# Performance work log

Measured on AMD Instinct MI355X. Metric: run time of the kernel, lower is better.

## Reference

```python
import jax, jax.numpy as jnp
import numpy as np

DIM = 1024
N_HEADS = 16
B, T = 2, 2048


def setup_inputs() -> dict:
    key = jax.random.key(0)
    ks = jax.random.split(key, 9)
    s = 1.0 / np.sqrt(DIM)
    return {
        "x": jax.random.normal(ks[0], (B, T, DIM), dtype=jnp.float32),
        "Wq": jax.random.normal(ks[1], (DIM, DIM), dtype=jnp.float32) * s,
        "bq": jnp.zeros((DIM,), dtype=jnp.float32),
        "Wk": jax.random.normal(ks[2], (DIM, DIM), dtype=jnp.float32) * s,
        "bk": jnp.zeros((DIM,), dtype=jnp.float32),
        "Wv": jax.random.normal(ks[3], (DIM, DIM), dtype=jnp.float32) * s,
        "bv": jnp.zeros((DIM,), dtype=jnp.float32),
        "Wo": jax.random.normal(ks[4], (DIM, DIM), dtype=jnp.float32) * s,
        "bo": jnp.zeros((DIM,), dtype=jnp.float32),
    }


def reference(x, Wq, bq, Wk, bk, Wv, bv, Wo, bo):
    Bv, Tv, d = x.shape
    n = N_HEADS
    hd = d // n
    # projections (torch Linear: x @ W.T + b)
    Q = x @ Wq.T + bq
    K = x @ Wk.T + bk
    V = x @ Wv.T + bv
    # [B, n, T, hd]
    Q = Q.reshape(Bv, Tv, n, hd).transpose(0, 2, 1, 3)
    K = K.reshape(Bv, Tv, n, hd).transpose(0, 2, 1, 3)
    V = V.reshape(Bv, Tv, n, hd).transpose(0, 2, 1, 3)
    # NOTE: original scales by full model dim, not head dim
    scale = 1.0 / jnp.sqrt(jnp.asarray(d, dtype=x.dtype))
    scores = jnp.einsum('bnqd,bnkd->bnqk', Q, K) * scale
    causal = jnp.tril(jnp.ones((Tv, Tv), dtype=bool))
    scores = jnp.where(causal, scores, jnp.asarray(-jnp.inf, dtype=scores.dtype))
    attn = jax.nn.softmax(scores, axis=-1)
    out = jnp.einsum('bnqk,bnkd->bnqd', attn, V)
    out = out.transpose(0, 2, 1, 3).reshape(Bv, Tv, d)
    return out @ Wo.T + bo
```

## Files before the change

### kernel.cpp

```cpp
#include <hip/hip_runtime.h>
#include <math.h>

#define DIMN 1024
#define NH 16
#define HD 64
#define BATCH 2
#define SEQ 2048
#define MROWS (BATCH*SEQ)

typedef unsigned short u16;
typedef unsigned int u32;
typedef __attribute__((ext_vector_type(8))) short bf16x8;
typedef __attribute__((ext_vector_type(4))) float f32x4;

__device__ __forceinline__ u16 f2bf(float f) {
    unsigned u = __float_as_uint(f);
    u += 0x7FFF + ((u >> 16) & 1);
    return (u16)(u >> 16);
}
__device__ __forceinline__ float bf2f(u16 s) {
    return __uint_as_float(((unsigned)s) << 16);
}

#define GLOADLDS16(g, s)                                                     \
    __builtin_amdgcn_global_load_lds(                                        \
        (const __attribute__((address_space(1))) void*)(g),                  \
        (__attribute__((address_space(3))) void*)(s), 16, 0, 0)

__global__ __launch_bounds__(256)
void split_hilo(const float* __restrict__ src, u16* __restrict__ h,
                u16* __restrict__ l, int n4)
{
    int i = blockIdx.x * 256 + threadIdx.x;
    if (i >= n4) return;
    float4 v = ((const float4*)src)[i];
    ushort4 hv, lv;
    hv.x = f2bf(v.x); lv.x = f2bf(v.x - bf2f(hv.x));
    hv.y = f2bf(v.y); lv.y = f2bf(v.y - bf2f(hv.y));
    hv.z = f2bf(v.z); lv.z = f2bf(v.z - bf2f(hv.z));
    hv.w = f2bf(v.w); lv.w = f2bf(v.w - bf2f(hv.w));
    ((ushort4*)h)[i] = hv;
    ((ushort4*)l)[i] = lv;
}

#define BM 128
#define BN 128
#define BK 32

template<bool QKV>
__global__ __launch_bounds__(256)
void mfma_gemm(const u16* __restrict__ Ah, const u16* __restrict__ Al,
               const u16* __restrict__ Wh0, const u16* __restrict__ Wl0,
               const u16* __restrict__ Wh1, const u16* __restrict__ Wl1,
               const u16* __restrict__ Wh2, const u16* __restrict__ Wl2,
               const float* __restrict__ b0, const float* __restrict__ b1,
               const float* __restrict__ b2,
               u16* __restrict__ Qh, u16* __restrict__ Ql,
               u16* __restrict__ Kh, u16* __restrict__ Kl,
               float* __restrict__ Vw, float* __restrict__ Yout)
{
    __shared__ u16 AhS[BM*BK], AlS[BM*BK], WhS[BN*BK], WlS[BN*BK];

    const u16* Wh = Wh0; const u16* Wl = Wl0; const float* bias = b0;
    if (QKV) {
        if (blockIdx.z == 1)      { Wh = Wh1; Wl = Wl1; bias = b1; }
        else if (blockIdx.z == 2) { Wh = Wh2; Wl = Wl2; bias = b2; }
    }

    const int tid  = threadIdx.x;
    const int lane = tid & 63;
    const int wid  = tid >> 6;
    const int wr   = wid >> 1;
    const int wc   = wid & 1;

    const int m0 = blockIdx.y * BM;
    const int n0 = blockIdx.x * BN;

    const int srow = lane >> 2;
    const int skc  = (lane & 3) << 3;
    const int c0 = wid * 2, c1 = wid * 2 + 1;
    const size_t aoffg0 = (size_t)(m0 + c0*16 + srow) * DIMN + skc;
    const size_t aoffg1 = (size_t)(m0 + c1*16 + srow) * DIMN + skc;
    const size_t woffg0 = (size_t)(n0 + c0*16 + srow) * DIMN + skc;
    const size_t woffg1 = (size_t)(n0 + c1*16 + srow) * DIMN + skc;

    f32x4 acc[4][4];
    #pragma unroll
    for (int m = 0; m < 4; ++m)
        #pragma unroll
        for (int n = 0; n < 4; ++n)
            acc[m][n] = (f32x4){0.f, 0.f, 0.f, 0.f};

    const int fr = lane & 15;
    const int fq = lane >> 4;
    const int aoff = (wr*64 + fr) * BK + fq*8;
    const int boff = (wc*64 + fr) * BK + fq*8;

    for (int k0 = 0; k0 < DIMN; k0 += BK) {
        GLOADLDS16(Ah + aoffg0 + k0, &AhS[c0*512]);
        GLOADLDS16(Ah + aoffg1 + k0, &AhS[c1*512]);
        GLOADLDS16(Al + aoffg0 + k0, &AlS[c0*512]);
        GLOADLDS16(Al + aoffg1 + k0, &AlS[c1*512]);
        GLOADLDS16(Wh + woffg0 + k0, &WhS[c0*512]);
        GLOADLDS16(Wh + woffg1 + k0, &WhS[c1*512]);
        GLOADLDS16(Wl + woffg0 + k0, &WlS[c0*512]);
        GLOADLDS16(Wl + woffg1 + k0, &WlS[c1*512]);
        __syncthreads();

        bf16x8 ah[4], al[4], bh[4], bl[4];
        #pragma unroll
        for (int m = 0; m < 4; ++m) {
            ah[m] = *(const bf16x8*)&AhS[aoff + m*16*BK];
            al[m] = *(const bf16x8*)&AlS[aoff + m*16*BK];
        }
        #pragma unroll
        for (int n = 0; n < 4; ++n) {
            bh[n] = *(const bf16x8*)&WhS[boff + n*16*BK];
            bl[n] = *(const bf16x8*)&WlS[boff + n*16*BK];
        }
        #pragma unroll
        for (int m = 0; m < 4; ++m)
            #pragma unroll
            for (int n = 0; n < 4; ++n) {
                acc[m][n] = __builtin_amdgcn_mfma_f32_16x16x32_bf16(ah[m], bh[n], acc[m][n], 0, 0, 0);
                acc[m][n] = __builtin_amdgcn_mfma_f32_16x16x32_bf16(ah[m], bl[n], acc[m][n], 0, 0, 0);
                acc[m][n] = __builtin_amdgcn_mfma_f32_16x16x32_bf16(al[m], bh[n], acc[m][n], 0, 0, 0);
            }
        __syncthreads();
    }

    #pragma unroll
    for (int n = 0; n < 4; ++n) {
        const int col = n0 + wc*64 + n*16 + fr;
        const float bv = bias[col];
        #pragma unroll
        for (int m = 0; m < 4; ++m) {
            #pragma unroll
            for (int j = 0; j < 4; ++j) {
                const int row = m0 + wr*64 + m*16 + fq*4 + j;
                float v = acc[m][n][j] + bv;
                if (QKV) {
                    const int b_ = row >> 11, t = row & (SEQ - 1);
                    const int hh = col >> 6, d = col & 63;
                    const size_t rb = (((size_t)b_*NH + hh)*SEQ + t)*HD;
                    if (blockIdx.z == 0) {
                        v *= 0.03125f;
                        u16 hv = f2bf(v), lv = f2bf(v - bf2f(hv));
                        Qh[rb + d] = hv; Ql[rb + d] = lv;
                    } else if (blockIdx.z == 1) {
                        u16 hv = f2bf(v), lv = f2bf(v - bf2f(hv));
                        const int ds = d ^ ((t & 7) << 3);
                        Kh[rb + ds] = hv; Kl[rb + ds] = lv;
                    } else {
                        Vw[rb + d] = v;
                    }
                } else {
                    Yout[(size_t)row*DIMN + col] = v;
                }
            }
        }
    }
}

__global__ __launch_bounds__(256)
void convV(const float* __restrict__ Vw, u16* __restrict__ Vth, u16* __restrict__ Vtl)
{
    __shared__ float Vs[64][68];
    const int tid = threadIdx.x;
    const int bh = blockIdx.y;
    const int t0 = blockIdx.x * 64;
    const float* src = Vw + ((size_t)bh*SEQ + t0)*HD;
    #pragma unroll
    for (int k = 0; k < 4; ++k) {
        int f4 = tid + k*256;
        int r = f4 >> 4, c4 = (f4 & 15) << 2;
        *(float4*)&Vs[r][c4] = *(const float4*)(src + (size_t)r*HD + c4);
    }
    __syncthreads();
    const int d  = tid >> 2;
    const int q2 = (tid & 3) << 4;
    u16* oh = Vth + ((size_t)bh*HD + d)*SEQ + t0;
    u16* ol = Vtl + ((size_t)bh*HD + d)*SEQ + t0;
    #pragma unroll
    for (int p = 0; p < 4; ++p) {
        const int lt = q2 + p*4;
        const int t_sw = (lt & 32) | ((((lt >> 3) & 3) ^ (d & 3)) << 3) | (lt & 7);
        ushort4 hv, lv; float v;
        v = Vs[lt + 0][d]; hv.x = f2bf(v); lv.x = f2bf(v - bf2f(hv.x));
        v = Vs[lt + 1][d]; hv.y = f2bf(v); lv.y = f2bf(v - bf2f(hv.y));
        v = Vs[lt + 2][d]; hv.z = f2bf(v); lv.z = f2bf(v - bf2f(hv.z));
        v = Vs[lt + 3][d]; hv.w = f2bf(v); lv.w = f2bf(v - bf2f(hv.w));
        *(ushort4*)(oh + t_sw) = hv;
        *(ushort4*)(ol + t_sw) = lv;
    }
}

__global__ __launch_bounds__(256)
void attn_mfma(const u16* __restrict__ Qhg, const u16* __restrict__ Qlg,
               const u16* __restrict__ Khg, const u16* __restrict__ Klg,
               const u16* __restrict__ Vthg, const u16* __restrict__ Vtlg,
               u16* __restrict__ AH, u16* __restrict__ AL)
{
    __shared__ u16 KVS[2][4][2048];
    __shared__ u16 PhS[4][640];
    __shared__ u16 PlS[4][640];

    const int tid  = threadIdx.x;
    const int lane = tid & 63;
    const int w    = tid >> 6;
    const int fr   = lane & 15;
    const int fq   = lane >> 4;
    const int bh   = blockIdx.y;
    const int b_   = bh >> 4;
    const int h    = bh & 15;

    auto stage = [&](int buf, int kt2) {
        u16* dst = &KVS[buf][w][0];
        if (w < 2) {
            const u16* g = (w == 0 ? Khg : Klg) +
                ((size_t)bh*SEQ + (size_t)kt2*32 + (lane>>3))*HD + ((lane&7)<<3);
            #pragma unroll
            for (int i = 0; i < 4; ++i)
                GLOADLDS16(g + (size_t)i*8*HD, dst + i*512);
        } else {
            const u16* g = (w == 2 ? Vthg : Vtlg) +
                ((size_t)bh*HD + (lane>>2))*SEQ + (size_t)kt2*32 + ((lane&3)<<3);
            #pragma unroll
            for (int i = 0; i < 4; ++i)
                GLOADLDS16(g + (size_t)i*16*SEQ, dst + i*512);
        }
    };

    #pragma unroll 1
    for (int pass = 0; pass < 2; ++pass) {
        const int qt   = pass ? (31 - blockIdx.x) : blockIdx.x;
        const int qabs = qt*64 + w*16 + fr;
        const int nt   = 2*qt + 2;

        bf16x8 qh[2], ql[2];
        {
            const size_t qrow = ((size_t)bh*SEQ + qabs)*HD;
            #pragma unroll
            for (int ks = 0; ks < 2; ++ks) {
                qh[ks] = *(const bf16x8*)&Qhg[qrow + ks*32 + (fq<<3)];
                ql[ks] = *(const bf16x8*)&Qlg[qrow + ks*32 + (fq<<3)];
            }
        }

        f32x4 o[4];
        #pragma unroll
        for (int md = 0; md < 4; ++md) o[md] = (f32x4){0.f,0.f,0.f,0.f};
        float mrun = -INFINITY, lrun = 0.f;

        __syncthreads();
        stage(0, 0);
        int cur = 0;

        for (int kt = 0; kt < nt; ++kt) {
            __syncthreads();
            if (kt + 1 < nt) stage(cur ^ 1, kt + 1);

            f32x4 s0 = (f32x4){0.f,0.f,0.f,0.f};
            f32x4 s1 = (f32x4){0.f,0.f,0.f,0.f};
            #pragma unroll
            for (int ks = 0; ks < 2; ++ks) {
                const int sl = (((ks*4 + fq) ^ (fr & 7)) << 3);
                bf16x8 a0h = *(const bf16x8*)&KVS[cur][0][fr*64 + sl];
                bf16x8 a0l = *(const bf16x8*)&KVS[cur][1][fr*64 + sl];
                bf16x8 a1h = *(const bf16x8*)&KVS[cur][0][(16+fr)*64 + sl];
                bf16x8 a1l = *(const bf16x8*)&KVS[cur][1][(16+fr)*64 + sl];
                s0 = __builtin_amdgcn_mfma_f32_16x16x32_bf16(a0h, qh[ks], s0, 0,0,0);
                s0 = __builtin_amdgcn_mfma_f32_16x16x32_bf16(a0h, ql[ks], s0, 0,0,0);
                s0 = __builtin_amdgcn_mfma_f32_16x16x32_bf16(a0l, qh[ks], s0, 0,0,0);
                s1 = __builtin_amdgcn_mfma_f32_16x16x32_bf16(a1h, qh[ks], s1, 0,0,0);
                s1 = __builtin_amdgcn_mfma_f32_16x16x32_bf16(a1h, ql[ks], s1, 0,0,0);
                s1 = __builtin_amdgcn_mfma_f32_16x16x32_bf16(a1l, qh[ks], s1, 0,0,0);
            }

            const int kb = kt*32 + fq*4;
            #pragma unroll
            for (int j = 0; j < 4; ++j) {
                if (kb + j      > qabs) s0[j] = -INFINITY;
                if (kb + 16 + j > qabs) s1[j] = -INFINITY;
            }

            float pm = fmaxf(fmaxf(fmaxf(s0[0],s0[1]), fmaxf(s0[2],s0[3])),
                             fmaxf(fmaxf(s1[0],s1[1]), fmaxf(s1[2],s1[3])));
            pm = fmaxf(pm, __shfl_xor(pm, 16));
            pm = fmaxf(pm, __shfl_xor(pm, 32));
            const float mnew = fmaxf(mrun, pm);
            const float fac  = __expf(mrun - mnew);
            float p[8];
            #pragma unroll
            for (int j = 0; j < 4; ++j) {
                p[j]   = __expf(s0[j] - mnew);
                p[4+j] = __expf(s1[j] - mnew);
            }
            float ls = ((p[0]+p[1]) + (p[2]+p[3])) + ((p[4]+p[5]) + (p[6]+p[7]));
            ls += __shfl_xor(ls, 16);
            ls += __shfl_xor(ls, 32);
            lrun = lrun * fac + ls;
            mrun = mnew;
            #pragma unroll
            for (int md = 0; md < 4; ++md) {
                o[md][0] *= fac; o[md][1] *= fac; o[md][2] *= fac; o[md][3] *= fac;
            }

            u16 ph[8], pl[8];
            #pragma unroll
            for (int i = 0; i < 8; ++i) {
                ph[i] = f2bf(p[i]);
                pl[i] = f2bf(p[i] - bf2f(ph[i]));
            }
            {
                const int pb = fr*40 + fq*4;
                uint2 w0, w1;
                w0.x = (u32)ph[0] | ((u32)ph[1] << 16);
                w0.y = (u32)ph[2] | ((u32)ph[3] << 16);
                w1.x = (u32)ph[4] | ((u32)ph[5] << 16);
                w1.y = (u32)ph[6] | ((u32)ph[7] << 16);
                *(uint2*)&PhS[w][pb]      = w0;
                *(uint2*)&PhS[w][pb + 16] = w1;
                w0.x = (u32)pl[0] | ((u32)pl[1] << 16);
                w0.y = (u32)pl[2] | ((u32)pl[3] << 16);
                w1.x = (u32)pl[4] | ((u32)pl[5] << 16);
                w1.y = (u32)pl[6] | ((u32)pl[7] << 16);
                *(uint2*)&PlS[w][pb]      = w0;
                *(uint2*)&PlS[w][pb + 16] = w1;
            }

            bf16x8 bph = *(const bf16x8*)&PhS[w][fr*40 + (fq<<3)];
            bf16x8 bpl = *(const bf16x8*)&PlS[w][fr*40 + (fq<<3)];
            #pragma unroll
            for (int md = 0; md < 4; ++md) {
                const int vsl = ((fq ^ (fr & 3)) << 3);
                bf16x8 avh = *(const bf16x8*)&KVS[cur][2][(md*16+fr)*32 + vsl];
                bf16x8 avl = *(const bf16x8*)&KVS[cur][3][(md*16+fr)*32 + vsl];
                o[md] = __builtin_amdgcn_mfma_f32_16x16x32_bf16(avh, bph, o[md], 0,0,0);
                o[md] = __builtin_amdgcn_mfma_f32_16x16x32_bf16(avh, bpl, o[md], 0,0,0);
                o[md] = __builtin_amdgcn_mfma_f32_16x16x32_bf16(avl, bph, o[md], 0,0,0);
            }
            cur ^= 1;
        }

        const float inv = 1.f / lrun;
        const size_t ob = ((size_t)b_*SEQ + qabs)*DIMN + h*64;
        #pragma unroll
        for (int md = 0; md < 4; ++md) {
            #pragma unroll
            for (int pr = 0; pr < 2; ++pr) {
                const int d0 = md*16 + fq*4 + pr*2;
                const float v0 = o[md][pr*2]   * inv;
                const float v1 = o[md][pr*2+1] * inv;
                u16 h0 = f2bf(v0), l0 = f2bf(v0 - bf2f(h0));
                u16 h1 = f2bf(v1), l1 = f2bf(v1 - bf2f(h1));
                *(u32*)&AH[ob + d0] = (u32)h0 | ((u32)h1 << 16);
                *(u32*)&AL[ob + d0] = (u32)l0 | ((u32)l1 << 16);
            }
        }
    }
}

extern "C" void kernel_launch(void* const* d_in, const int* in_sizes, int n_in,
                              void* d_out, int out_size, void* d_ws, size_t ws_size,
                              hipStream_t stream)
{
    const float* x  = (const float*)d_in[0];
    const float* Wq = (const float*)d_in[1];
    const float* bq = (const float*)d_in[2];
    const float* Wk = (const float*)d_in[3];
    const float* bk = (const float*)d_in[4];
    const float* Wv = (const float*)d_in[5];
    const float* bv = (const float*)d_in[6];
    const float* Wo = (const float*)d_in[7];
    const float* bo = (const float*)d_in[8];
    float* out = (float*)d_out;

    const size_t NX = (size_t)MROWS * DIMN;
    const size_t NW = (size_t)DIMN * DIMN;

    u16* Xh  = (u16*)d_ws;
    u16* Xl  = Xh  + NX;
    u16* WhQ = Xl  + NX;
    u16* WlQ = WhQ + NW;
    u16* WhK = WlQ + NW;
    u16* WlK = WhK + NW;
    u16* WhV = WlK + NW;
    u16* WlV = WhV + NW;
    u16* WhO = WlV + NW;
    u16* WlO = WhO + NW;
    u16* Qh  = WlO + NW;
    u16* Ql  = Qh + NX;
    u16* Kh  = Ql + NX;
    u16* Kl  = Kh + NX;
    u16* Vth = Kl + NX;
    u16* Vtl = Vth + NX;
    float* Vw = (float*)(Vtl + NX);
    u16* AH = Xh;
    u16* AL = Xl;

    const int n4x = (int)(NX / 4);
    const int n4w = (int)(NW / 4);
    split_hilo<<<n4x/256, 256, 0, stream>>>(x,  Xh,  Xl,  n4x);
    split_hilo<<<n4w/256, 256, 0, stream>>>(Wq, WhQ, WlQ, n4w);
    split_hilo<<<n4w/256, 256, 0, stream>>>(Wk, WhK, WlK, n4w);
    split_hilo<<<n4w/256, 256, 0, stream>>>(Wv, WhV, WlV, n4w);
    split_hilo<<<n4w/256, 256, 0, stream>>>(Wo, WhO, WlO, n4w);

    dim3 gq(DIMN / BN, MROWS / BM, 3);
    mfma_gemm<true><<<gq, 256, 0, stream>>>(Xh, Xl, WhQ, WlQ, WhK, WlK, WhV, WlV,
                                            bq, bk, bv, Qh, Ql, Kh, Kl, Vw, nullptr);

    dim3 gv(SEQ / 64, BATCH * NH);
    convV<<<gv, 256, 0, stream>>>(Vw, Vth, Vtl);

    dim3 ga(16, BATCH * NH);
    attn_mfma<<<ga, 256, 0, stream>>>(Qh, Ql, Kh, Kl, Vth, Vtl, AH, AL);

    dim3 gp(DIMN / BN, MROWS / BM, 1);
    mfma_gemm<false><<<gp, 256, 0, stream>>>(AH, AL, WhO, WlO, nullptr, nullptr,
                                             nullptr, nullptr, bo, nullptr, nullptr,
                                             nullptr, nullptr, nullptr, nullptr,
                                             nullptr, out);
}
```

Before: 380.2 us.

## Pre-pack operands into MFMA fragment order and drop LDS staging in GEMMs

The hi/lo bf16 split kernel now writes x and the weights in a packed layout that matches the MFMA 16x32 fragment order. Each wave can then load its fragments straight from global memory with contiguous 16-byte loads, so the GEMM no longer stages through LDS and no longer needs the block barriers. The attention kernel now writes fp32 output, and a separate pack pass converts it before the output projection, which uses a narrower 4x2 fragment tile per wave to give a larger grid. This adds an extra pass over the attention output. It also gives up LDS reuse between the waves of a block, so more traffic must be served by L2.

```diff
diff --git a/kernel.cpp b/kernel.cpp
--- a/kernel.cpp
+++ b/kernel.cpp
@@ -7,6 +7,7 @@
 #define BATCH 2
 #define SEQ 2048
 #define MROWS (BATCH*SEQ)
+#define NKB   (DIMN/32)
 
 typedef unsigned short u16;
 typedef unsigned int u32;
@@ -28,43 +29,50 @@
         (__attribute__((address_space(3))) void*)(s), 16, 0, 0)
 
 __global__ __launch_bounds__(256)
-void split_hilo(const float* __restrict__ src, u16* __restrict__ h,
-                u16* __restrict__ l, int n4)
+void pack_hilo(const float* __restrict__ src, u16* __restrict__ dh,
+               u16* __restrict__ dl, int ngran)
 {
-    int i = blockIdx.x * 256 + threadIdx.x;
-    if (i >= n4) return;
-    float4 v = ((const float4*)src)[i];
-    ushort4 hv, lv;
-    hv.x = f2bf(v.x); lv.x = f2bf(v.x - bf2f(hv.x));
-    hv.y = f2bf(v.y); lv.y = f2bf(v.y - bf2f(hv.y));
-    hv.z = f2bf(v.z); lv.z = f2bf(v.z - bf2f(hv.z));
-    hv.w = f2bf(v.w); lv.w = f2bf(v.w - bf2f(hv.w));
-    ((ushort4*)h)[i] = hv;
-    ((ushort4*)l)[i] = lv;
-}
-
-#define BM 128
-#define BN 128
-#define BK 32
-
-template<bool QKV>
+    int g = blockIdx.x * 256 + threadIdx.x;
+    if (g >= ngran) return;
+    const int lane = g & 63;
+    const int kb   = (g >> 6) & (NKB - 1);
+    const int rb   = g >> 11;
+    const int row  = rb * 16 + (lane & 15);
+    const int col  = kb * 32 + (lane >> 4) * 8;
+    const float* s = src + (size_t)row * DIMN + col;
+    float4 v0 = *(const float4*)s;
+    float4 v1 = *(const float4*)(s + 4);
+    ushort4 h0, h1, l0, l1;
+    h0.x = f2bf(v0.x); l0.x = f2bf(v0.x - bf2f(h0.x));
+    h0.y = f2bf(v0.y); l0.y = f2bf(v0.y - bf2f(h0.y));
+    h0.z = f2bf(v0.z); l0.z = f2bf(v0.z - bf2f(h0.z));
+    h0.w = f2bf(v0.w); l0.w = f2bf(v0.w - bf2f(h0.w));
+    h1.x = f2bf(v1.x); l1.x = f2bf(v1.x - bf2f(h1.x));
+    h1.y = f2bf(v1.y); l1.y = f2bf(v1.y - bf2f(h1.y));
+    h1.z = f2bf(v1.z); l1.z = f2bf(v1.z - bf2f(h1.z));
+    h1.w = f2bf(v1.w); l1.w = f2bf(v1.w - bf2f(h1.w));
+    *(ushort4*)(dh + (size_t)g * 8)     = h0;
+    *(ushort4*)(dh + (size_t)g * 8 + 4) = h1;
+    *(ushort4*)(dl + (size_t)g * 8)     = l0;
+    *(ushort4*)(dl + (size_t)g * 8 + 4) = l1;
+}
+
+template<int MF, int NF, bool QKV>
 __global__ __launch_bounds__(256)
-void mfma_gemm(const u16* __restrict__ Ah, const u16* __restrict__ Al,
-               const u16* __restrict__ Wh0, const u16* __restrict__ Wl0,
-               const u16* __restrict__ Wh1, const u16* __restrict__ Wl1,
-               const u16* __restrict__ Wh2, const u16* __restrict__ Wl2,
-               const float* __restrict__ b0, const float* __restrict__ b1,
-               const float* __restrict__ b2,
-               u16* __restrict__ Qh, u16* __restrict__ Ql,
-               u16* __restrict__ Kh, u16* __restrict__ Kl,
-               float* __restrict__ Vw, float* __restrict__ Yout)
+void pgemm(const u16* __restrict__ Aph, const u16* __restrict__ Apl,
+           const u16* __restrict__ Wph0, const u16* __restrict__ Wpl0,
+           const u16* __restrict__ Wph1, const u16* __restrict__ Wpl1,
+           const u16* __restrict__ Wph2, const u16* __restrict__ Wpl2,
+           const float* __restrict__ b0, const float* __restrict__ b1,
+           const float* __restrict__ b2,
+           u16* __restrict__ Qh, u16* __restrict__ Ql,
+           u16* __restrict__ Kh, u16* __restrict__ Kl,
+           float* __restrict__ Vw, float* __restrict__ Yout)
 {
-    __shared__ u16 AhS[BM*BK], AlS[BM*BK], WhS[BN*BK], WlS[BN*BK];
-
-    const u16* Wh = Wh0; const u16* Wl = Wl0; const float* bias = b0;
+    const u16* Wph = Wph0; const u16* Wpl = Wpl0; const float* bias = b0;
     if (QKV) {
-        if (blockIdx.z == 1)      { Wh = Wh1; Wl = Wl1; bias = b1; }
-        else if (blockIdx.z == 2) { Wh = Wh2; Wl = Wl2; bias = b2; }
+        if (blockIdx.z == 1)      { Wph = Wph1; Wpl = Wpl1; bias = b1; }
+        else if (blockIdx.z == 2) { Wph = Wph2; Wpl = Wpl2; bias = b2; }
     }
 
     const int tid  = threadIdx.x;
@@ -72,72 +80,55 @@
     const int wid  = tid >> 6;
     const int wr   = wid >> 1;
     const int wc   = wid & 1;
-
-    const int m0 = blockIdx.y * BM;
-    const int n0 = blockIdx.x * BN;
-
-    const int srow = lane >> 2;
-    const int skc  = (lane & 3) << 3;
-    const int c0 = wid * 2, c1 = wid * 2 + 1;
-    const size_t aoffg0 = (size_t)(m0 + c0*16 + srow) * DIMN + skc;
-    const size_t aoffg1 = (size_t)(m0 + c1*16 + srow) * DIMN + skc;
-    const size_t woffg0 = (size_t)(n0 + c0*16 + srow) * DIMN + skc;
-    const size_t woffg1 = (size_t)(n0 + c1*16 + srow) * DIMN + skc;
-
-    f32x4 acc[4][4];
+    const int mb0  = blockIdx.y * (2*MF) + wr*MF;
+    const int nb0  = blockIdx.x * (2*NF) + wc*NF;
+
+    const u16* Ah = Aph + (size_t)mb0 * (NKB*512) + lane*8;
+    const u16* Al = Apl + (size_t)mb0 * (NKB*512) + lane*8;
+    const u16* Bh = Wph + (size_t)nb0 * (NKB*512) + lane*8;
+    const u16* Bl = Wpl + (size_t)nb0 * (NKB*512) + lane*8;
+
+    f32x4 acc[MF][NF];
     #pragma unroll
-    for (int m = 0; m < 4; ++m)
-        #pragma unroll
-        for (int n = 0; n < 4; ++n)
+    for (int m = 0; m < MF; ++m)
+        #pragma unroll
+        for (int n = 0; n < NF; ++n)
             acc[m][n] = (f32x4){0.f, 0.f, 0.f, 0.f};
 
-    const int fr = lane & 15;
-    const int fq = lane >> 4;
-    const int aoff = (wr*64 + fr) * BK + fq*8;
-    const int boff = (wc*64 + fr) * BK + fq*8;
-
-    for (int k0 = 0; k0 < DIMN; k0 += BK) {
-        GLOADLDS16(Ah + aoffg0 + k0, &AhS[c0*512]);
-        GLOADLDS16(Ah + aoffg1 + k0, &AhS[c1*512]);
-        GLOADLDS16(Al + aoffg0 + k0, &AlS[c0*512]);
-        GLOADLDS16(Al + aoffg1 + k0, &AlS[c1*512]);
-        GLOADLDS16(Wh + woffg0 + k0, &WhS[c0*512]);
-        GLOADLDS16(Wh + woffg1 + k0, &WhS[c1*512]);
-        GLOADLDS16(Wl + woffg0 + k0, &WlS[c0*512]);
-        GLOADLDS16(Wl + woffg1 + k0, &WlS[c1*512]);
-        __syncthreads();
-
-        bf16x8 ah[4], al[4], bh[4], bl[4];
-        #pragma unroll
-        for (int m = 0; m < 4; ++m) {
-            ah[m] = *(const bf16x8*)&AhS[aoff + m*16*BK];
-            al[m] = *(const bf16x8*)&AlS[aoff + m*16*BK];
-        }
-        #pragma unroll
-        for (int n = 0; n < 4; ++n) {
-            bh[n] = *(const bf16x8*)&WhS[boff + n*16*BK];
-            bl[n] = *(const bf16x8*)&WlS[boff + n*16*BK];
-        }
-        #pragma unroll
-        for (int m = 0; m < 4; ++m)
-            #pragma unroll
-            for (int n = 0; n < 4; ++n) {
+    for (int kb = 0; kb < NKB; ++kb) {
+        const int ko = kb * 512;
+        bf16x8 ah[MF], al[MF], bh[NF], bl[NF];
+        #pragma unroll
+        for (int m = 0; m < MF; ++m) {
+            ah[m] = *(const bf16x8*)(Ah + ko + m*(NKB*512));
+            al[m] = *(const bf16x8*)(Al + ko + m*(NKB*512));
+        }
+        #pragma unroll
+        for (int n = 0; n < NF; ++n) {
+            bh[n] = *(const bf16x8*)(Bh + ko + n*(NKB*512));
+            bl[n] = *(const bf16x8*)(Bl + ko + n*(NKB*512));
+        }
+        #pragma unroll
+        for (int m = 0; m < MF; ++m)
+            #pragma unroll
+            for (int n = 0; n < NF; ++n) {
                 acc[m][n] = __builtin_amdgcn_mfma_f32_16x16x32_bf16(ah[m], bh[n], acc[m][n], 0, 0, 0);
                 acc[m][n] = __builtin_amdgcn_mfma_f32_16x16x32_bf16(ah[m], bl[n], acc[m][n], 0, 0, 0);
                 acc[m][n] = __builtin_amdgcn_mfma_f32_16x16x32_bf16(al[m], bh[n], acc[m][n], 0, 0, 0);
             }
-        __syncthreads();
-    }
-
+    }
+
+    const int fr = lane & 15;
+    const int fq = lane >> 4;
     #pragma unroll
-    for (int n = 0; n < 4; ++n) {
-        const int col = n0 + wc*64 + n*16 + fr;
+    for (int n = 0; n < NF; ++n) {
+        const int col = (nb0 + n)*16 + fr;
         const float bv = bias[col];
         #pragma unroll
-        for (int m = 0; m < 4; ++m) {
+        for (int m = 0; m < MF; ++m) {
             #pragma unroll
             for (int j = 0; j < 4; ++j) {
-                const int row = m0 + wr*64 + m*16 + fq*4 + j;
+                const int row = (mb0 + m)*16 + fq*4 + j;
                 float v = acc[m][n][j] + bv;
                 if (QKV) {
                     const int b_ = row >> 11, t = row & (SEQ - 1);
@@ -199,7 +190,7 @@
 void attn_mfma(const u16* __restrict__ Qhg, const u16* __restrict__ Qlg,
                const u16* __restrict__ Khg, const u16* __restrict__ Klg,
                const u16* __restrict__ Vthg, const u16* __restrict__ Vtlg,
-               u16* __restrict__ AH, u16* __restrict__ AL)
+               float* __restrict__ Oc)
 {
     __shared__ u16 KVS[2][4][2048];
     __shared__ u16 PhS[4][640];
@@ -344,19 +335,13 @@
         }
 
         const float inv = 1.f / lrun;
-        const size_t ob = ((size_t)b_*SEQ + qabs)*DIMN + h*64;
+        float* dst = Oc + ((size_t)b_*SEQ + qabs)*DIMN + h*64;
         #pragma unroll
         for (int md = 0; md < 4; ++md) {
-            #pragma unroll
-            for (int pr = 0; pr < 2; ++pr) {
-                const int d0 = md*16 + fq*4 + pr*2;
-                const float v0 = o[md][pr*2]   * inv;
-                const float v1 = o[md][pr*2+1] * inv;
-                u16 h0 = f2bf(v0), l0 = f2bf(v0 - bf2f(h0));
-                u16 h1 = f2bf(v1), l1 = f2bf(v1 - bf2f(h1));
-                *(u32*)&AH[ob + d0] = (u32)h0 | ((u32)h1 << 16);
-                *(u32*)&AL[ob + d0] = (u32)l0 | ((u32)l1 << 16);
-            }
+            float4 v;
+            v.x = o[md][0]*inv; v.y = o[md][1]*inv;
+            v.z = o[md][2]*inv; v.w = o[md][3]*inv;
+            *(float4*)(dst + md*16 + fq*4) = v;
         }
     }
 }
@@ -379,47 +364,44 @@
     const size_t NX = (size_t)MROWS * DIMN;
     const size_t NW = (size_t)DIMN * DIMN;
 
-    u16* Xh  = (u16*)d_ws;
-    u16* Xl  = Xh  + NX;
-    u16* WhQ = Xl  + NX;
-    u16* WlQ = WhQ + NW;
-    u16* WhK = WlQ + NW;
-    u16* WlK = WhK + NW;
-    u16* WhV = WlK + NW;
-    u16* WlV = WhV + NW;
-    u16* WhO = WlV + NW;
-    u16* WlO = WhO + NW;
-    u16* Qh  = WlO + NW;
+    u16* Xph = (u16*)d_ws;
+    u16* Xpl = Xph + NX;
+    u16* WpQh = Xpl + NX;  u16* WpQl = WpQh + NW;
+    u16* WpKh = WpQl + NW; u16* WpKl = WpKh + NW;
+    u16* WpVh = WpKl + NW; u16* WpVl = WpVh + NW;
+    u16* WpOh = WpVl + NW; u16* WpOl = WpOh + NW;
+    u16* Qh  = WpOl + NW;
     u16* Ql  = Qh + NX;
     u16* Kh  = Ql + NX;
     u16* Kl  = Kh + NX;
     u16* Vth = Kl + NX;
     u16* Vtl = Vth + NX;
     float* Vw = (float*)(Vtl + NX);
-    u16* AH = Xh;
-    u16* AL = Xl;
-
-    const int n4x = (int)(NX / 4);
-    const int n4w = (int)(NW / 4);
-    split_hilo<<<n4x/256, 256, 0, stream>>>(x,  Xh,  Xl,  n4x);
-    split_hilo<<<n4w/256, 256, 0, stream>>>(Wq, WhQ, WlQ, n4w);
-    split_hilo<<<n4w/256, 256, 0, stream>>>(Wk, WhK, WlK, n4w);
-    split_hilo<<<n4w/256, 256, 0, stream>>>(Wv, WhV, WlV, n4w);
-    split_hilo<<<n4w/256, 256, 0, stream>>>(Wo, WhO, WlO, n4w);
-
-    dim3 gq(DIMN / BN, MROWS / BM, 3);
-    mfma_gemm<true><<<gq, 256, 0, stream>>>(Xh, Xl, WhQ, WlQ, WhK, WlK, WhV, WlV,
-                                            bq, bk, bv, Qh, Ql, Kh, Kl, Vw, nullptr);
+
+    const int ngx = (int)(NX / 8);
+    const int ngw = (int)(NW / 8);
+    pack_hilo<<<ngx/256, 256, 0, stream>>>(x,  Xph, Xpl, ngx);
+    pack_hilo<<<ngw/256, 256, 0, stream>>>(Wq, WpQh, WpQl, ngw);
+    pack_hilo<<<ngw/256, 256, 0, stream>>>(Wk, WpKh, WpKl, ngw);
+    pack_hilo<<<ngw/256, 256, 0, stream>>>(Wv, WpVh, WpVl, ngw);
+    pack_hilo<<<ngw/256, 256, 0, stream>>>(Wo, WpOh, WpOl, ngw);
+
+    dim3 gq(DIMN/128, MROWS/128, 3);
+    pgemm<4,4,true><<<gq, 256, 0, stream>>>(Xph, Xpl,
+        WpQh, WpQl, WpKh, WpKl, WpVh, WpVl, bq, bk, bv,
+        Qh, Ql, Kh, Kl, Vw, nullptr);
 
     dim3 gv(SEQ / 64, BATCH * NH);
     convV<<<gv, 256, 0, stream>>>(Vw, Vth, Vtl);
 
+    float* Oc = Vw;
     dim3 ga(16, BATCH * NH);
-    attn_mfma<<<ga, 256, 0, stream>>>(Qh, Ql, Kh, Kl, Vth, Vtl, AH, AL);
-
-    dim3 gp(DIMN / BN, MROWS / BM, 1);
-    mfma_gemm<false><<<gp, 256, 0, stream>>>(AH, AL, WhO, WlO, nullptr, nullptr,
-                                             nullptr, nullptr, bo, nullptr, nullptr,
-                                             nullptr, nullptr, nullptr, nullptr,
-                                             nullptr, out);
-}
+    attn_mfma<<<ga, 256, 0, stream>>>(Qh, Ql, Kh, Kl, Vth, Vtl, Oc);
+
+    pack_hilo<<<ngx/256, 256, 0, stream>>>(Oc, Xph, Xpl, ngx);
+
+    dim3 gp(DIMN/64, MROWS/128, 1);
+    pgemm<4,2,false><<<gp, 256, 0, stream>>>(Xph, Xpl,
+        WpOh, WpOl, nullptr, nullptr, nullptr, nullptr, bo, nullptr, nullptr,
+        nullptr, nullptr, nullptr, nullptr, nullptr, out);
+}
```

Result: slower. 412.4 us (+8.5%).
